# Performance work log

Measured on AMD Instinct MI355X. Metric: run time of the kernel, lower is better.

Reference implementation:

```python
import jax, jax.numpy as jnp
import numpy as np

B = 256      # batch size
N = 8192     # neurons per layer (uniform layer width)
E = 262144   # edges per layer (avg in-degree 32)
L = 4        # number of edge layers


def setup_inputs() -> dict:
    key = jax.random.key(0)
    k_x, k_src, k_dst, k_w = jax.random.split(key, 4)
    x = jax.random.normal(k_x, (B, N), dtype=jnp.float32)
    edge_src = jax.random.randint(k_src, (L, E), 0, N)  # source neuron in prev layer
    edge_dst = jax.random.randint(k_dst, (L, E), 0, N)  # dest neuron in curr layer
    # torch init: randn(num_edges) * sqrt(2 / (prev_size + curr_size))
    w_scale = float(np.sqrt(2.0 / (N + N)))
    weights = jax.random.normal(k_w, (L, E), dtype=jnp.float32) * w_scale
    bias = jnp.zeros((L, N), dtype=jnp.float32)  # torch.zeros init
    return {"x": x, "weights": weights, "bias": bias,
            "edge_src": edge_src, "edge_dst": edge_dst}


def reference(x, weights, bias, edge_src, edge_dst):
    """Per layer: gather(src) * w -> scatter_add(dst) -> + bias -> relu."""
    out = x  # [B, N]
    for l in range(L):  # small fixed number of structurally distinct layers
        src = edge_src[l]          # [E]
        dst = edge_dst[l]          # [E]
        gathered = out[:, src] * weights[l]  # [B, E] weighted source activations
        # scatter_add over destination neurons (duplicates accumulate)
        agg = jax.ops.segment_sum(gathered.T, dst, num_segments=N).T  # [B, N]
        out = jax.nn.relu(agg + bias[l])
    return out
```

## Files before the change

### kernel.cpp

```cpp
#include <hip/hip_runtime.h>


static constexpr int BATCH = 256;
static constexpr int NN    = 8192;
static constexpr int NE    = 262144;
static constexpr int NL    = 4;
static constexpr int NBUK  = 128;
static constexpr int BCAP  = 3072;
static constexpr int CHUNK = 2048;

__device__ inline unsigned bf16rne(float f) {
  unsigned u = __float_as_uint(f);
  return (u + 0x7fffu + ((u >> 16) & 1u)) >> 16;
}
__device__ inline float bf16tof(unsigned us) { return __uint_as_float(us << 16); }
__device__ inline float blo(unsigned u) { return __uint_as_float(u << 16); }
__device__ inline float bhi(unsigned u) { return __uint_as_float(u & 0xffff0000u); }

__global__ void transpose_in_k(const float* __restrict__ in, ushort* __restrict__ out,
                               int* __restrict__ bcur) {
  if (blockIdx.x == 0 && blockIdx.y == 0) {
    int t = threadIdx.y * 32 + threadIdx.x;
    for (int i = t; i < NL * NBUK; i += 256) bcur[i] = 0;
  }
  __shared__ float tile[32][33];
  int c0 = blockIdx.x * 32, r0 = blockIdx.y * 32;
  int tx = threadIdx.x, ty = threadIdx.y;
#pragma unroll
  for (int i = ty; i < 32; i += 8)
    tile[i][tx] = in[(size_t)(r0 + i) * NN + (c0 + tx)];
  __syncthreads();
#pragma unroll
  for (int i = ty; i < 32; i += 8)
    out[(size_t)(c0 + i) * BATCH + (r0 + tx)] = (ushort)bf16rne(tile[tx][i]);
}

__global__ void transpose_out_k(const ushort* __restrict__ in, float* __restrict__ out) {
  __shared__ float tile[32][33];
  int c0 = blockIdx.x * 32, r0 = blockIdx.y * 32;
  int tx = threadIdx.x, ty = threadIdx.y;
#pragma unroll
  for (int i = ty; i < 32; i += 8)
    tile[i][tx] = bf16tof(in[(size_t)(r0 + i) * BATCH + (c0 + tx)]);
  __syncthreads();
#pragma unroll
  for (int i = ty; i < 32; i += 8)
    out[(size_t)(c0 + i) * NN + (r0 + tx)] = tile[tx][i];
}

__global__ void part_k(const int* __restrict__ src, const int* __restrict__ dst,
                       const float* __restrict__ w, int* __restrict__ bcur,
                       uint2* __restrict__ stag) {
  __shared__ int cnt[NBUK], sc[NBUK], loff[NBUK], gbase[NBUK], lcur[NBUK];
  __shared__ uint2 ebuf[CHUNK];
  __shared__ unsigned char bkt[CHUNK];
  int t = threadIdx.x;
  int l = blockIdx.x >> 7;
  size_t e0 = (size_t)blockIdx.x * CHUNK;
  if (t < NBUK) cnt[t] = 0;
  __syncthreads();
  int es[8], ed[8]; float ew[8];
#pragma unroll
  for (int k = 0; k < 8; ++k) {
    size_t e = e0 + t + k * 256;
    es[k] = src[e]; ed[k] = dst[e]; ew[k] = w[e];
    atomicAdd(&cnt[ed[k] >> 6], 1);
  }
  __syncthreads();
  if (t < NBUK) sc[t] = cnt[t];
  __syncthreads();
  for (int off = 1; off < NBUK; off <<= 1) {
    int v = 0;
    if (t < NBUK && t >= off) v = sc[t - off];
    __syncthreads();
    if (t < NBUK) sc[t] += v;
    __syncthreads();
  }
  if (t < NBUK) {
    int excl = sc[t] - cnt[t];
    loff[t] = excl;
    lcur[t] = excl;
    gbase[t] = atomicAdd(&bcur[(l << 7) + t], cnt[t]);
  }
  __syncthreads();
#pragma unroll
  for (int k = 0; k < 8; ++k) {
    int b = ed[k] >> 6;
    int p = atomicAdd(&lcur[b], 1);
    ebuf[p] = make_uint2((unsigned)es[k] | ((unsigned)(ed[k] & 63) << 16),
                         __float_as_uint(ew[k]));
    bkt[p]  = (unsigned char)b;
  }
  __syncthreads();
#pragma unroll
  for (int k = 0; k < 8; ++k) {
    int i = t + k * 256;
    int b = bkt[i];
    int gp = gbase[b] + (i - loff[b]);
    if ((unsigned)gp < BCAP)
      stag[(size_t)((l << 7) + b) * BCAP + gp] = ebuf[i];
  }
}

__global__ void place_k(const uint2* __restrict__ stag, const int* __restrict__ bcur,
                        float2* __restrict__ csr, int* __restrict__ rp) {
  __shared__ int bc[NBUK], bsc[NBUK];
  __shared__ int cnt[64], sc64[64], lcur[64];
  __shared__ uint2 ebuf[BCAP];
  int t = threadIdx.x;
  int gb = blockIdx.x, l = gb >> 7, b = gb & 127;
  if (t < NBUK) { bc[t] = min(bcur[(l << 7) + t], BCAP); bsc[t] = bc[t]; }
  if (t < 64) cnt[t] = 0;
  __syncthreads();
  for (int off = 1; off < NBUK; off <<= 1) {
    int v = 0;
    if (t < NBUK && t >= off) v = bsc[t - off];
    __syncthreads();
    if (t < NBUK) bsc[t] += v;
    __syncthreads();
  }
  int n   = bc[b];
  int seg = bsc[b] - bc[b];
  for (int i = t; i < n; i += 256)
    ebuf[i] = stag[(size_t)gb * BCAP + i];
  __syncthreads();
  for (int i = t; i < n; i += 256)
    atomicAdd(&cnt[(ebuf[i].x >> 16) & 63], 1);
  __syncthreads();
  if (t < 64) sc64[t] = cnt[t];
  __syncthreads();
  for (int off = 1; off < 64; off <<= 1) {
    int v = 0;
    if (t < 64 && t >= off) v = sc64[t - off];
    __syncthreads();
    if (t < 64) sc64[t] += v;
    __syncthreads();
  }
  if (t < 64) {
    int excl = sc64[t] - cnt[t];
    lcur[t] = excl;
    rp[l * (NN + 1) + (b << 6) + t] = seg + excl;
  }
  if (b == 127 && t == 65) rp[l * (NN + 1) + NN] = bsc[127];
  __syncthreads();
  for (int i = t; i < n; i += 256) {
    uint2 r = ebuf[i];
    int p = atomicAdd(&lcur[(r.x >> 16) & 63], 1);
    csr[(size_t)l * NE + seg + p] =
        make_float2(__int_as_float((int)(r.x & 0xffffu)), __uint_as_float(r.y));
  }
}

__global__ __launch_bounds__(256) void
gather_k(const ushort* __restrict__ act, ushort* __restrict__ out,
         const float2* __restrict__ csr, const int* __restrict__ rp,
         const float* __restrict__ bias) {
  __shared__ unsigned long long smeta[4][64];
  int wid  = threadIdx.x >> 6;
  int row  = blockIdx.x * 4 + wid;
  int lane = threadIdx.x & 63;
  int half = lane >> 5;
  int l32  = lane & 31;
  int k0 = rp[row], k1 = rp[row + 1];
  float4 accA = make_float4(0.f, 0.f, 0.f, 0.f);
  float4 accB = make_float4(0.f, 0.f, 0.f, 0.f);
  const ushort* actc = act + l32 * 8;
  const unsigned long long* mp = &smeta[wid][half];
  for (int kc = k0; kc < k1; kc += 64) {
    int nk = k1 - kc;
    if (nk > 64) nk = 64;
    int ksel = lane < nk ? lane : 0;
    unsigned long long mu =
        __builtin_nontemporal_load((const unsigned long long*)(csr + kc + ksel));
    if (lane >= nk) mu = 0ull;
    smeta[wid][lane] = mu;
    int npair = (nk + 1) >> 1;
#pragma unroll 8
    for (int j = 0; j < npair; ++j) {
      unsigned long long m = mp[2 * j];
      int   s  = (int)(m & 0xffffffffu);
      float wt = __uint_as_float((unsigned)(m >> 32));
      uint4 v = *(const uint4*)(actc + (size_t)s * BATCH);
      accA.x += wt * blo(v.x); accA.y += wt * bhi(v.x);
      accA.z += wt * blo(v.y); accA.w += wt * bhi(v.y);
      accB.x += wt * blo(v.z); accB.y += wt * bhi(v.z);
      accB.z += wt * blo(v.w); accB.w += wt * bhi(v.w);
    }
  }
  accA.x += __shfl(accA.x, lane ^ 32); accA.y += __shfl(accA.y, lane ^ 32);
  accA.z += __shfl(accA.z, lane ^ 32); accA.w += __shfl(accA.w, lane ^ 32);
  accB.x += __shfl(accB.x, lane ^ 32); accB.y += __shfl(accB.y, lane ^ 32);
  accB.z += __shfl(accB.z, lane ^ 32); accB.w += __shfl(accB.w, lane ^ 32);
  if (half == 0) {
    float b = bias[row];
    uint4 o;
    o.x = bf16rne(fmaxf(accA.x + b, 0.f)) | (bf16rne(fmaxf(accA.y + b, 0.f)) << 16);
    o.y = bf16rne(fmaxf(accA.z + b, 0.f)) | (bf16rne(fmaxf(accA.w + b, 0.f)) << 16);
    o.z = bf16rne(fmaxf(accB.x + b, 0.f)) | (bf16rne(fmaxf(accB.y + b, 0.f)) << 16);
    o.w = bf16rne(fmaxf(accB.z + b, 0.f)) | (bf16rne(fmaxf(accB.w + b, 0.f)) << 16);
    *(uint4*)(out + (size_t)row * BATCH + l32 * 8) = o;
  }
}

extern "C" void kernel_launch(void* const* d_in, const int* in_sizes, int n_in,
                              void* d_out, int out_size, void* d_ws, size_t ws_size,
                              hipStream_t stream) {
  const float* x       = (const float*)d_in[0];
  const float* weights = (const float*)d_in[1];
  const float* bias    = (const float*)d_in[2];
  const int*   esrc    = (const int*)d_in[3];
  const int*   edst    = (const int*)d_in[4];
  float*       out     = (float*)d_out;

  char* p = (char*)d_ws;
  float2* csr     = (float2*)p; p += (size_t)NL * NE * 8;
  int*    row_ptr = (int*)p;    p += (size_t)NL * (NN + 1) * 4;
  int*    bcur    = (int*)p;    p += (size_t)NL * NBUK * 4;
  uint2*  stag    = (uint2*)p;  p += (size_t)NL * NBUK * BCAP * 8;
  ushort* actA    = (ushort*)p; p += (size_t)NN * BATCH * 2;
  ushort* actB    = (ushort*)p;

  transpose_in_k<<<dim3(NN / 32, BATCH / 32), dim3(32, 8), 0, stream>>>(x, actA, bcur);

  part_k<<<(NL * NE) / CHUNK, 256, 0, stream>>>(esrc, edst, weights, bcur, stag);
  place_k<<<NL * NBUK, 256, 0, stream>>>(stag, bcur, csr, row_ptr);

  for (int l = 0; l < NL; ++l) {
    gather_k<<<NN / 4, 256, 0, stream>>>((l & 1) ? actB : actA,
                                         (l & 1) ? actA : actB,
                                         csr + (size_t)l * NE,
                                         row_ptr + (size_t)l * (NN + 1),
                                         bias + (size_t)l * NN);
  }

  transpose_out_k<<<dim3(BATCH / 32, NN / 32), dim3(32, 8), 0, stream>>>(actA, out);
}
```

Baseline: 90.16 us.

## Split batch into 64-column slices and process 8 edges per wave iteration

The gather kernel now gives each block one 64-wide batch slice across 16 rows. Each wave handles 4 rows in turn, and each of its 8 lane groups handles a different edge while reading 128 bytes of that edge's source activation slice. Partial sums are then combined with xor shuffles across the 8 groups. This spreads more independent gathers across lanes per iteration to raise memory-level parallelism. In exchange it adds shuffle-reduction work and re-reads the CSR metadata once for each of the 4 slices.

New measurement: 126.4 us. +40.2%, slower.

```diff
diff --git a/kernel.cpp b/kernel.cpp
--- a/kernel.cpp
+++ b/kernel.cpp
@@ -156,49 +156,56 @@
          const float2* __restrict__ csr, const int* __restrict__ rp,
          const float* __restrict__ bias) {
   __shared__ unsigned long long smeta[4][64];
-  int wid  = threadIdx.x >> 6;
-  int row  = blockIdx.x * 4 + wid;
-  int lane = threadIdx.x & 63;
-  int half = lane >> 5;
-  int l32  = lane & 31;
-  int k0 = rp[row], k1 = rp[row + 1];
-  float4 accA = make_float4(0.f, 0.f, 0.f, 0.f);
-  float4 accB = make_float4(0.f, 0.f, 0.f, 0.f);
-  const ushort* actc = act + l32 * 8;
-  const unsigned long long* mp = &smeta[wid][half];
-  for (int kc = k0; kc < k1; kc += 64) {
-    int nk = k1 - kc;
-    if (nk > 64) nk = 64;
-    int ksel = lane < nk ? lane : 0;
-    unsigned long long mu =
-        __builtin_nontemporal_load((const unsigned long long*)(csr + kc + ksel));
-    if (lane >= nk) mu = 0ull;
-    smeta[wid][lane] = mu;
-    int npair = (nk + 1) >> 1;
-#pragma unroll 8
-    for (int j = 0; j < npair; ++j) {
-      unsigned long long m = mp[2 * j];
-      int   s  = (int)(m & 0xffffffffu);
-      float wt = __uint_as_float((unsigned)(m >> 32));
-      uint4 v = *(const uint4*)(actc + (size_t)s * BATCH);
-      accA.x += wt * blo(v.x); accA.y += wt * bhi(v.x);
-      accA.z += wt * blo(v.y); accA.w += wt * bhi(v.y);
-      accB.x += wt * blo(v.z); accB.y += wt * bhi(v.z);
-      accB.z += wt * blo(v.w); accB.w += wt * bhi(v.w);
+  int wid   = threadIdx.x >> 6;
+  int lane  = threadIdx.x & 63;
+  int slot  = lane >> 3;
+  int q     = lane & 7;
+  int slice = blockIdx.x & 3;
+  int rbase = ((blockIdx.x >> 2) * 4 + wid) * 4;
+  const ushort* actc = act + slice * 64 + q * 8;
+  const unsigned long long* mp = &smeta[wid][slot];
+  for (int r = 0; r < 4; ++r) {
+    int row = rbase + r;
+    int k0 = rp[row], k1 = rp[row + 1];
+    float a0 = 0.f, a1 = 0.f, a2 = 0.f, a3 = 0.f;
+    float a4 = 0.f, a5 = 0.f, a6 = 0.f, a7 = 0.f;
+    for (int kc = k0; kc < k1; kc += 64) {
+      int nk = k1 - kc;
+      if (nk > 64) nk = 64;
+      int ksel = lane < nk ? lane : 0;
+      unsigned long long mu =
+          __builtin_nontemporal_load((const unsigned long long*)(csr + kc + ksel));
+      if (lane >= nk) mu = 0ull;
+      smeta[wid][lane] = mu;
+      int niter = (nk + 7) >> 3;
+#pragma unroll 4
+      for (int j = 0; j < niter; ++j) {
+        unsigned long long m = mp[j * 8];
+        int   s  = (int)(m & 0xffffffffu);
+        float wt = __uint_as_float((unsigned)(m >> 32));
+        uint4 v = *(const uint4*)(actc + (size_t)s * BATCH);
+        a0 += wt * blo(v.x); a1 += wt * bhi(v.x);
+        a2 += wt * blo(v.y); a3 += wt * bhi(v.y);
+        a4 += wt * blo(v.z); a5 += wt * bhi(v.z);
+        a6 += wt * blo(v.w); a7 += wt * bhi(v.w);
+      }
     }
-  }
-  accA.x += __shfl(accA.x, lane ^ 32); accA.y += __shfl(accA.y, lane ^ 32);
-  accA.z += __shfl(accA.z, lane ^ 32); accA.w += __shfl(accA.w, lane ^ 32);
-  accB.x += __shfl(accB.x, lane ^ 32); accB.y += __shfl(accB.y, lane ^ 32);
-  accB.z += __shfl(accB.z, lane ^ 32); accB.w += __shfl(accB.w, lane ^ 32);
-  if (half == 0) {
-    float b = bias[row];
-    uint4 o;
-    o.x = bf16rne(fmaxf(accA.x + b, 0.f)) | (bf16rne(fmaxf(accA.y + b, 0.f)) << 16);
-    o.y = bf16rne(fmaxf(accA.z + b, 0.f)) | (bf16rne(fmaxf(accA.w + b, 0.f)) << 16);
-    o.z = bf16rne(fmaxf(accB.x + b, 0.f)) | (bf16rne(fmaxf(accB.y + b, 0.f)) << 16);
-    o.w = bf16rne(fmaxf(accB.z + b, 0.f)) | (bf16rne(fmaxf(accB.w + b, 0.f)) << 16);
-    *(uint4*)(out + (size_t)row * BATCH + l32 * 8) = o;
+#pragma unroll
+    for (int msk = 8; msk < 64; msk <<= 1) {
+      a0 += __shfl_xor(a0, msk); a1 += __shfl_xor(a1, msk);
+      a2 += __shfl_xor(a2, msk); a3 += __shfl_xor(a3, msk);
+      a4 += __shfl_xor(a4, msk); a5 += __shfl_xor(a5, msk);
+      a6 += __shfl_xor(a6, msk); a7 += __shfl_xor(a7, msk);
+    }
+    if (slot == 0) {
+      float b = bias[row];
+      uint4 o;
+      o.x = bf16rne(fmaxf(a0 + b, 0.f)) | (bf16rne(fmaxf(a1 + b, 0.f)) << 16);
+      o.y = bf16rne(fmaxf(a2 + b, 0.f)) | (bf16rne(fmaxf(a3 + b, 0.f)) << 16);
+      o.z = bf16rne(fmaxf(a4 + b, 0.f)) | (bf16rne(fmaxf(a5 + b, 0.f)) << 16);
+      o.w = bf16rne(fmaxf(a6 + b, 0.f)) | (bf16rne(fmaxf(a7 + b, 0.f)) << 16);
+      *(uint4*)(out + (size_t)row * BATCH + slice * 64 + q * 8) = o;
+    }
   }
 }
 
@@ -226,11 +233,11 @@
   place_k<<<NL * NBUK, 256, 0, stream>>>(stag, bcur, csr, row_ptr);
 
   for (int l = 0; l < NL; ++l) {
-    gather_k<<<NN / 4, 256, 0, stream>>>((l & 1) ? actB : actA,
-                                         (l & 1) ? actA : actB,
-                                         csr + (size_t)l * NE,
-                                         row_ptr + (size_t)l * (NN + 1),
-                                         bias + (size_t)l * NN);
+    gather_k<<<2048, 256, 0, stream>>>((l & 1) ? actB : actA,
+                                       (l & 1) ? actA : actB,
+                                       csr + (size_t)l * NE,
+                                       row_ptr + (size_t)l * (NN + 1),
+                                       bias + (size_t)l * NN);
   }
 
   transpose_out_k<<<dim3(BATCH / 32, NN / 32), dim3(32, 8), 0, stream>>>(actA, out);
```
